# Kernel optimization log

Measured on AMD Instinct MI355X. Metric: run time of the kernel, lower is better.

Reference implementation:

```python
import jax, jax.numpy as jnp
import numpy as np

N = 100_000      # nodes
E = 3_200_000    # directed edges (avg degree 32)
F_IN = 503
C = 32           # GATConv out_channels, heads=1
NEG_SLOPE = 0.2  # PyG GATConv default


def setup_inputs() -> dict:
    key = jax.random.key(0)
    ks = jax.random.split(key, 14)
    x = jax.random.normal(ks[0], (N, F_IN), jnp.float32)
    edge_index = jax.random.randint(ks[1], (2, E), 0, N)
    edge_weight = jax.random.uniform(ks[2], (E, 1), jnp.float32)
    input_mask = jnp.ones((N, 1), jnp.float32)
    # GATConv params (heads=1)
    W_src = jax.random.normal(ks[3], (C, F_IN), jnp.float32) * 0.02
    att_src = jax.random.normal(ks[4], (C,), jnp.float32) * 0.1
    att_dst = jax.random.normal(ks[5], (C,), jnp.float32) * 0.1
    att_edge = jax.random.normal(ks[6], (C,), jnp.float32) * 0.1
    W_edge = jax.random.normal(ks[7], (C, 1), jnp.float32) * 0.1
    bias_conv = jnp.zeros((C,), jnp.float32)
    # dense heads
    Wb = jax.random.normal(ks[8], (1, C), jnp.float32) * 0.1
    bb = jnp.zeros((1,), jnp.float32)
    Ww = jax.random.normal(ks[9], (1, C), jnp.float32) * 0.1
    bw = jnp.zeros((1,), jnp.float32)
    return {"x": x, "edge_index": edge_index, "edge_weight": edge_weight,
            "input_mask": input_mask, "W_src": W_src, "att_src": att_src,
            "att_dst": att_dst, "att_edge": att_edge, "W_edge": W_edge,
            "bias_conv": bias_conv, "Wb": Wb, "bb": bb, "Ww": Ww, "bw": bw}


def reference(x, edge_index, edge_weight, input_mask, W_src, att_src, att_dst,
              att_edge, W_edge, bias_conv, Wb, bb, Ww, bw):
    n = x.shape[0]
    xl = x @ W_src.T                       # [N, C] transformed node features
    a_src = xl @ att_src                   # [N] per-node source attention logit
    a_dst = xl @ att_dst                   # [N]
    src, dst = edge_index[0], edge_index[1]
    # add_self_loops=True with fill_value='mean' for edge_attr (PyG default)
    loop = jnp.arange(n)
    mean_attr = jnp.mean(edge_weight, axis=0, keepdims=True)      # [1,1]
    ea = jnp.concatenate([edge_weight, jnp.broadcast_to(mean_attr, (n, 1))], 0)
    s = jnp.concatenate([src, loop])       # [E+N]
    d = jnp.concatenate([dst, loop])
    a_edge = (ea @ W_edge.T) @ att_edge    # [E+N]
    alpha = jax.nn.leaky_relu(a_src[s] + a_dst[d] + a_edge, NEG_SLOPE)
    # softmax over incoming edges of each destination node
    amax = jax.ops.segment_max(alpha, d, num_segments=n)
    ex = jnp.exp(alpha - amax[d])
    denom = jax.ops.segment_sum(ex, d, num_segments=n)
    w = ex / denom[d]                      # [E+N] attention coeffs
    msg = xl[s] * w[:, None]               # [E+N, C]
    out = jax.ops.segment_sum(msg, d, num_segments=n) + bias_conv  # [N, C]
    h = jax.nn.relu(out)
    biases = (h @ Wb.T + bb) * input_mask  # [N, 1]
    weights = ((h[src] + h[dst]) * 0.5) @ Ww.T + bw  # [E, 1]
    return weights, biases
```

## Files before the change

### kernel.cpp

```cpp
#include <hip/hip_runtime.h>
#include <stdint.h>

#define NN 100000
#define NE 3200000
#define FIN 503
#define COUT 32
#define NSLOPE 0.2f

#define BSH 6
#define NB 1563
#define HB 256
#define EPB (NE / HB)
#define NSB 7
#define MAXBE 2560

typedef __bf16 bf16x8 __attribute__((ext_vector_type(8)));
typedef float  f32x4  __attribute__((ext_vector_type(4)));

__device__ __forceinline__ unsigned short bf1(float f) {
    unsigned u = __float_as_uint(f);
    u = (u + 0x7FFFu + ((u >> 16) & 1u)) >> 16;
    return (unsigned short)u;
}
__device__ __forceinline__ unsigned bf2(float a, float b) {
    return (unsigned)bf1(a) | ((unsigned)bf1(b) << 16);
}
__device__ __forceinline__ float unbf(unsigned short h) {
    return __uint_as_float(((unsigned)h) << 16);
}

__global__ __launch_bounds__(256)
void k_pre(const int* __restrict__ ei_dst, const float* __restrict__ ew,
           const float* __restrict__ W, uint4* __restrict__ wfrag,
           float* __restrict__ partial, unsigned* __restrict__ part,
           unsigned* __restrict__ done)
{
    __shared__ unsigned h[NB];
    __shared__ float wsum[4];
    const int t = threadIdx.x;
    const int b = blockIdx.x;
    const int gid = b * 256 + t;

    if (gid == 0) *done = 0u;
    for (int i = t; i < NB; i += 256) h[i] = 0u;

    if (gid < 2048) {
        int c = gid & 31;
        int quad = (gid >> 5) & 3;
        int chunk = gid >> 7;
        int kb = chunk * 32 + quad * 8;
        float v[8];
        #pragma unroll
        for (int j = 0; j < 8; ++j) {
            int k = kb + j;
            v[j] = (k < FIN) ? W[c * FIN + k] : 0.f;
        }
        uint4 o;
        o.x = bf2(v[0], v[1]); o.y = bf2(v[2], v[3]);
        o.z = bf2(v[4], v[5]); o.w = bf2(v[6], v[7]);
        wfrag[gid] = o;
    }
    __syncthreads();

    const int base = b * EPB;
    for (int i = t; i < EPB; i += 256)
        atomicAdd(&h[ei_dst[base + i] >> BSH], 1u);

    const float4* ew4 = (const float4*)ew;
    float s = 0.f;
    for (int i = gid; i < NE / 4; i += HB * 256) {
        float4 v = ew4[i];
        s += v.x + v.y + v.z + v.w;
    }
    #pragma unroll
    for (int off = 32; off > 0; off >>= 1) s += __shfl_xor(s, off);
    if ((t & 63) == 0) wsum[t >> 6] = s;
    __syncthreads();
    if (t == 0) partial[b] = wsum[0] + wsum[1] + wsum[2] + wsum[3];
    for (int i = t; i < NB; i += 256)
        part[(size_t)b * NB + i] = h[i];
}

#define GR 64

__global__ __launch_bounds__(256)
void k_gemm(const float* __restrict__ x, const uint4* __restrict__ wfrag,
            const float* __restrict__ att_s, const float* __restrict__ att_d,
            unsigned short* __restrict__ xlb,
            float* __restrict__ a_src, float* __restrict__ a_dst)
{
    __shared__ __align__(16) float xs[2][GR][36];
    unsigned short* os = (unsigned short*)&xs[0][0][0];
    const int t = threadIdx.x;
    const int wv = t >> 6, lane = t & 63;
    const int m16 = lane & 15, quad = lane >> 4;
    const int row0 = blockIdx.x * GR;
    const int srow = t >> 5;
    const int scol = t & 31;
    const int rowf = wv * 16 + m16;

    auto stage = [&](int ch, int buf) {
        const int k = ch * 32 + scol;
        const bool ok = (k < FIN);
        #pragma unroll
        for (int p = 0; p < 8; ++p) {
            int r = p * 8 + srow;
            int rg = row0 + r;
            rg = (rg < NN) ? rg : (NN - 1);
            xs[buf][r][scol] = ok ? x[(size_t)rg * FIN + k] : 0.f;
        }
    };

    f32x4 acc0 = {0.f, 0.f, 0.f, 0.f};
    f32x4 acc1 = {0.f, 0.f, 0.f, 0.f};

    stage(0, 0);
    for (int ch = 0; ch < 16; ++ch) {
        __syncthreads();
        if (ch < 15) stage(ch + 1, (ch + 1) & 1);
        float av[8];
        *(f32x4*)&av[0] = *(const f32x4*)&xs[ch & 1][rowf][quad * 8];
        *(f32x4*)&av[4] = *(const f32x4*)&xs[ch & 1][rowf][quad * 8 + 4];
        bf16x8 af;
        #pragma unroll
        for (int j = 0; j < 8; ++j) af[j] = (__bf16)av[j];
        uint4 b0 = wfrag[ch * 128 + quad * 32 + m16];
        uint4 b1 = wfrag[ch * 128 + quad * 32 + 16 + m16];
        acc0 = __builtin_amdgcn_mfma_f32_16x16x32_bf16(af, *(bf16x8*)&b0, acc0, 0, 0, 0);
        acc1 = __builtin_amdgcn_mfma_f32_16x16x32_bf16(af, *(bf16x8*)&b1, acc1, 0, 0, 0);
    }

    #pragma unroll
    for (int r = 0; r < 4; ++r) {
        int rr = wv * 16 + quad * 4 + r;
        os[rr * 40 + m16]      = bf1(acc0[r]);
        os[rr * 40 + 16 + m16] = bf1(acc1[r]);
    }
    __syncthreads();
    {
        int r = t >> 2, c0 = (t & 3) * 8;
        int grow = row0 + r;
        uint4 o = *(const uint4*)&os[r * 40 + c0];
        float s = 0.f, dd = 0.f;
        const unsigned short* oh = (const unsigned short*)&o;
        #pragma unroll
        for (int j = 0; j < 8; ++j) {
            float v = unbf(oh[j]);
            s  += v * att_s[c0 + j];
            dd += v * att_d[c0 + j];
        }
        s  += __shfl_xor(s, 1, 4);  s  += __shfl_xor(s, 2, 4);
        dd += __shfl_xor(dd, 1, 4); dd += __shfl_xor(dd, 2, 4);
        if (grow < NN) {
            *(uint4*)&xlb[(size_t)grow * COUT + c0] = o;
            if ((t & 3) == 0) { a_src[grow] = s; a_dst[grow] = dd; }
        }
    }
}

__global__ __launch_bounds__(256)
void k_scan(unsigned* __restrict__ part, unsigned* __restrict__ colsum,
            unsigned* __restrict__ done, const float* __restrict__ partial,
            const float* __restrict__ W_edge, const float* __restrict__ att_e,
            float* __restrict__ stats, unsigned* __restrict__ bbase)
{
    const int t = threadIdx.x;
    const int bkt = blockIdx.x * 256 + t;
    if (bkt < NB) {
        unsigned run = 0u;
        #pragma unroll 1
        for (int s = 0; s < HB; s += 4) {
            unsigned v0 = part[(size_t)(s    ) * NB + bkt];
            unsigned v1 = part[(size_t)(s + 1) * NB + bkt];
            unsigned v2 = part[(size_t)(s + 2) * NB + bkt];
            unsigned v3 = part[(size_t)(s + 3) * NB + bkt];
            part[(size_t)(s    ) * NB + bkt] = run; run += v0;
            part[(size_t)(s + 1) * NB + bkt] = run; run += v1;
            part[(size_t)(s + 2) * NB + bkt] = run; run += v2;
            part[(size_t)(s + 3) * NB + bkt] = run; run += v3;
        }
        colsum[bkt] = run;
    }
    __threadfence();
    __syncthreads();
    __shared__ unsigned winner;
    if (t == 0) winner = atomicAdd(done, 1u);
    __syncthreads();
    if (winner != NSB - 1) return;

    __shared__ float fs[256];
    fs[t] = partial[t];
    __syncthreads();
    for (int off = 128; off > 0; off >>= 1) {
        if (t < off) fs[t] += fs[t + off];
        __syncthreads();
    }
    if (t == 0) {
        stats[0] = fs[0];
        float k = 0.f;
        for (int c = 0; c < COUT; ++c) k += W_edge[c] * att_e[c];
        stats[1] = k;
    }
    __syncthreads();
    __shared__ unsigned sm[256];
    __shared__ unsigned carry;
    if (t == 0) carry = 0u;
    __syncthreads();
    for (int c0 = 0; c0 < NB; c0 += 256) {
        int i = c0 + t;
        unsigned cv = (i < NB) ? atomicAdd(&colsum[i], 0u) : 0u;
        sm[t] = cv;
        for (int off = 1; off < 256; off <<= 1) {
            __syncthreads();
            unsigned tv = (t >= off) ? sm[t - off] : 0u;
            __syncthreads();
            sm[t] += tv;
        }
        __syncthreads();
        if (i < NB) bbase[i] = carry + sm[t] - cv;
        __syncthreads();
        if (t == 0) carry += sm[255];
        __syncthreads();
    }
    if (t == 0) bbase[NB] = carry;
}

__global__ __launch_bounds__(512)
void k_scatter(const int* __restrict__ ei, const float* __restrict__ ew,
               const float* __restrict__ a_src, const float* __restrict__ stats,
               const unsigned* __restrict__ part, const unsigned* __restrict__ bbase,
               uint2* __restrict__ csr)
{
    __shared__ unsigned cur[NB];
    const int b = blockIdx.x;
    const int t = threadIdx.x;
    for (int i = t; i < NB; i += 512)
        cur[i] = bbase[i] + part[(size_t)b * NB + i];
    __syncthreads();
    const float kc = stats[1];
    const int base = b * EPB;
    for (int i = t; i < EPB; i += 512) {
        int e = base + i;
        int s = ei[e];
        int d = ei[NE + e];
        float pre = a_src[s] + kc * ew[e];
        unsigned pos = atomicAdd(&cur[d >> BSH], 1u);
        csr[pos] = make_uint2((unsigned)s | ((unsigned)(d & 63) << 20),
                              __float_as_uint(pre));
    }
}

__global__ __launch_bounds__(256)
void k_aggr(const uint2* __restrict__ csr, const unsigned* __restrict__ bbase,
            const float* __restrict__ a_src, const float* __restrict__ a_dst,
            const unsigned short* __restrict__ xlb, const float* __restrict__ stats,
            const float* __restrict__ bias_conv, const float* __restrict__ Wb,
            const float* __restrict__ bb, const float* __restrict__ Ww,
            const float* __restrict__ mask, float* __restrict__ out_b,
            float* __restrict__ hw)
{
    __shared__ uint2 rec[MAXBE];
    __shared__ unsigned seg[65], cur[64];
    const int t = threadIdx.x;
    const int b = blockIdx.x;
    const int jb = (int)bbase[b];
    int ne = (int)bbase[b + 1] - jb;
    if (ne > MAXBE) ne = MAXBE;

    if (t < 64) cur[t] = 0u;
    __syncthreads();
    for (int i = t; i < ne; i += 256)
        atomicAdd(&cur[csr[jb + i].x >> 20], 1u);
    __syncthreads();
    if (t < 64) {
        unsigned v = cur[t];
        unsigned s = v;
        #pragma unroll
        for (int off = 1; off < 64; off <<= 1) {
            unsigned u = __shfl_up(s, off, 64);
            if (t >= off) s += u;
        }
        seg[t + 1] = s;
        cur[t] = s - v;
        if (t == 0) seg[0] = 0u;
    }
    __syncthreads();
    for (int i = t; i < ne; i += 256) {
        uint2 r = csr[jb + i];
        unsigned pos = atomicAdd(&cur[r.x >> 20], 1u);
        rec[pos] = r;
    }
    __syncthreads();

    const float kmean = stats[1] * (stats[0] * (1.f / NE));
    const int lane = t & 31;
    for (int dl = t >> 5; dl < 64; dl += 8) {
        int d = (b << BSH) + dl;
        if (d >= NN) continue;
        const float adv = a_dst[d];
        float a0 = a_src[d] + adv + kmean;
        a0 = (a0 > 0.f) ? a0 : NSLOPE * a0;
        const float ps = __expf(a0);
        float l = 0.f;
        float acc = ps * unbf(xlb[(size_t)d * COUT + lane]);
        const int j0 = (int)seg[dl], j1 = (int)seg[dl + 1];
        for (int tb = j0; tb < j1; tb += 32) {
            int j = tb + lane;
            float p = 0.f;
            if (j < j1) {
                uint2 en = rec[j];
                float a = __uint_as_float(en.y) + adv;
                a = (a > 0.f) ? a : NSLOPE * a;
                p = __expf(a);
                rec[j].y = __float_as_uint(p);
            }
            l += p;
            int cnte = min(32, j1 - tb);
            #pragma unroll 4
            for (int k = 0; k < cnte; ++k) {
                uint2 en = rec[tb + k];
                acc += __uint_as_float(en.y) *
                       unbf(xlb[(size_t)(en.x & 0xFFFFFu) * COUT + lane]);
            }
        }
        #pragma unroll
        for (int off = 16; off > 0; off >>= 1) l += __shfl_xor(l, off, 32);
        l += ps;
        float h = fmaxf(acc / l + bias_conv[lane], 0.f);
        float pb = h * Wb[lane];
        float pw = h * Ww[lane];
        #pragma unroll
        for (int off = 16; off > 0; off >>= 1) {
            pb += __shfl_xor(pb, off, 32);
            pw += __shfl_xor(pw, off, 32);
        }
        if (lane == 0) {
            out_b[d] = (pb + bb[0]) * mask[d];
            hw[d] = pw;
        }
    }
}

__global__ void k_weights(const int* __restrict__ ei, const float* __restrict__ hw,
                          const float* __restrict__ bw, float* __restrict__ out_w)
{
    int e4 = blockIdx.x * 256 + threadIdx.x;
    if (e4 < NE / 4) {
        int4 s4 = ((const int4*)ei)[e4];
        int4 d4 = ((const int4*)(ei + NE))[e4];
        float bwv = bw[0];
        float4 o;
        o.x = 0.5f * (hw[s4.x] + hw[d4.x]) + bwv;
        o.y = 0.5f * (hw[s4.y] + hw[d4.y]) + bwv;
        o.z = 0.5f * (hw[s4.z] + hw[d4.z]) + bwv;
        o.w = 0.5f * (hw[s4.w] + hw[d4.w]) + bwv;
        ((float4*)out_w)[e4] = o;
    }
}

extern "C" void kernel_launch(void* const* d_in, const int* in_sizes, int n_in,
                              void* d_out, int out_size, void* d_ws, size_t ws_size,
                              hipStream_t stream)
{
    const float* x        = (const float*)d_in[0];
    const int*   ei       = (const int*)d_in[1];
    const float* ew       = (const float*)d_in[2];
    const float* mask     = (const float*)d_in[3];
    const float* W_src    = (const float*)d_in[4];
    const float* att_src  = (const float*)d_in[5];
    const float* att_dst  = (const float*)d_in[6];
    const float* att_edge = (const float*)d_in[7];
    const float* W_edge   = (const float*)d_in[8];
    const float* bias_c   = (const float*)d_in[9];
    const float* Wb       = (const float*)d_in[10];
    const float* bb       = (const float*)d_in[11];
    const float* Ww       = (const float*)d_in[12];
    const float* bw       = (const float*)d_in[13];
    (void)in_sizes; (void)n_in; (void)out_size; (void)ws_size;

    char* wsp = (char*)d_ws;
    size_t off = 0;
    auto alloc = [&](size_t bytes) -> void* {
        void* p = wsp + off;
        off = (off + bytes + 255) & ~(size_t)255;
        return p;
    };
    unsigned short* xlb    = (unsigned short*)alloc((size_t)NN * COUT * 2);
    uint4*    wfrag  = (uint4*)alloc(2048 * 16);
    float*    a_src  = (float*)alloc((size_t)NN * 4);
    float*    a_dst  = (float*)alloc((size_t)NN * 4);
    float*    stats  = (float*)alloc(256);
    float*    partial= (float*)alloc((size_t)HB * 4);
    unsigned* part   = (unsigned*)alloc((size_t)HB * NB * 4);
    unsigned* colsum = (unsigned*)alloc((size_t)NB * 4);
    unsigned* bbase  = (unsigned*)alloc((size_t)(NB + 1) * 4);
    unsigned* done   = (unsigned*)alloc(256);
    uint2*    csr    = (uint2*)alloc((size_t)NE * 8);
    float*    hw     = (float*)alloc((size_t)NN * 4);

    float* out_w = (float*)d_out;
    float* out_b = out_w + NE;

    k_pre     <<<HB, 256, 0, stream>>>(ei + NE, ew, W_src, wfrag, partial, part, done);
    k_gemm    <<<(NN + GR - 1) / GR, 256, 0, stream>>>(x, wfrag, att_src, att_dst,
                                                       xlb, a_src, a_dst);
    k_scan    <<<NSB, 256, 0, stream>>>(part, colsum, done, partial, W_edge,
                                        att_edge, stats, bbase);
    k_scatter <<<HB, 512, 0, stream>>>(ei, ew, a_src, stats, part, bbase, csr);
    k_aggr    <<<NB, 256, 0, stream>>>(csr, bbase, a_src, a_dst, xlb, stats,
                                       bias_c, Wb, bb, Ww, mask, out_b, hw);
    k_weights <<<NE / 4 / 256, 256, 0, stream>>>(ei, hw, bw, out_w);
}
```

Measured before the change: 561.9 us.

## Fuse histogram prepass into GEMM kernel and widen histogram partitioning

Merges the histogram/edge-weight-sum prepass and the feature GEMM into one launch: the first blocks do the GEMM, loading W rows directly from global memory and converting them to bf16, while the extra blocks build per-block destination histograms. This drops a kernel launch and the wfrag staging buffer, and lets the histogram work overlap with the GEMM. The histogram/scatter partition count is doubled to 512 blocks of 256 threads, which doubles the size of the scan's partial-count array and the per-block bucket initialisation cost in the scatter kernel. Each GEMM wave now issues strided per-element loads of W instead of reading pre-packed fragments.

Result: slower. 573.5 us (+2.0%).

```diff
diff --git a/kernel.cpp b/kernel.cpp
--- a/kernel.cpp
+++ b/kernel.cpp
@@ -9,8 +9,9 @@
 
 #define BSH 6
 #define NB 1563
-#define HB 256
-#define EPB (NE / HB)
+#define NGB 1563
+#define NHB 512
+#define EPB (NE / NHB)
 #define NSB 7
 #define MAXBE 2560
 
@@ -22,82 +23,59 @@
     u = (u + 0x7FFFu + ((u >> 16) & 1u)) >> 16;
     return (unsigned short)u;
 }
-__device__ __forceinline__ unsigned bf2(float a, float b) {
-    return (unsigned)bf1(a) | ((unsigned)bf1(b) << 16);
-}
 __device__ __forceinline__ float unbf(unsigned short h) {
     return __uint_as_float(((unsigned)h) << 16);
 }
 
+#define GR 64
+
 __global__ __launch_bounds__(256)
-void k_pre(const int* __restrict__ ei_dst, const float* __restrict__ ew,
-           const float* __restrict__ W, uint4* __restrict__ wfrag,
-           float* __restrict__ partial, unsigned* __restrict__ part,
-           unsigned* __restrict__ done)
-{
-    __shared__ unsigned h[NB];
-    __shared__ float wsum[4];
+void k_fused1(const float* __restrict__ x, const float* __restrict__ W,
+              const float* __restrict__ att_s, const float* __restrict__ att_d,
+              unsigned short* __restrict__ xlb,
+              float* __restrict__ a_src, float* __restrict__ a_dst,
+              const int* __restrict__ ei_dst, const float* __restrict__ ew,
+              float* __restrict__ partial, unsigned* __restrict__ part,
+              unsigned* __restrict__ done)
+{
+    __shared__ __align__(16) float xs[2][GR][36];
     const int t = threadIdx.x;
-    const int b = blockIdx.x;
-    const int gid = b * 256 + t;
-
-    if (gid == 0) *done = 0u;
-    for (int i = t; i < NB; i += 256) h[i] = 0u;
-
-    if (gid < 2048) {
-        int c = gid & 31;
-        int quad = (gid >> 5) & 3;
-        int chunk = gid >> 7;
-        int kb = chunk * 32 + quad * 8;
-        float v[8];
-        #pragma unroll
-        for (int j = 0; j < 8; ++j) {
-            int k = kb + j;
-            v[j] = (k < FIN) ? W[c * FIN + k] : 0.f;
-        }
-        uint4 o;
-        o.x = bf2(v[0], v[1]); o.y = bf2(v[2], v[3]);
-        o.z = bf2(v[4], v[5]); o.w = bf2(v[6], v[7]);
-        wfrag[gid] = o;
-    }
-    __syncthreads();
-
-    const int base = b * EPB;
-    for (int i = t; i < EPB; i += 256)
-        atomicAdd(&h[ei_dst[base + i] >> BSH], 1u);
-
-    const float4* ew4 = (const float4*)ew;
-    float s = 0.f;
-    for (int i = gid; i < NE / 4; i += HB * 256) {
-        float4 v = ew4[i];
-        s += v.x + v.y + v.z + v.w;
-    }
-    #pragma unroll
-    for (int off = 32; off > 0; off >>= 1) s += __shfl_xor(s, off);
-    if ((t & 63) == 0) wsum[t >> 6] = s;
-    __syncthreads();
-    if (t == 0) partial[b] = wsum[0] + wsum[1] + wsum[2] + wsum[3];
-    for (int i = t; i < NB; i += 256)
-        part[(size_t)b * NB + i] = h[i];
-}
-
-#define GR 64
-
-__global__ __launch_bounds__(256)
-void k_gemm(const float* __restrict__ x, const uint4* __restrict__ wfrag,
-            const float* __restrict__ att_s, const float* __restrict__ att_d,
-            unsigned short* __restrict__ xlb,
-            float* __restrict__ a_src, float* __restrict__ a_dst)
-{
-    __shared__ __align__(16) float xs[2][GR][36];
+
+    if (blockIdx.x >= NGB) {
+        unsigned* h = (unsigned*)&xs[0][0][0];
+        __shared__ float wsum[4];
+        const int hb = blockIdx.x - NGB;
+        for (int i = t; i < NB; i += 256) h[i] = 0u;
+        __syncthreads();
+        const int base = hb * EPB;
+        for (int i = t; i < EPB; i += 256)
+            atomicAdd(&h[ei_dst[base + i] >> BSH], 1u);
+        const float4* ew4 = (const float4*)ew;
+        float s = 0.f;
+        for (int i = hb * 256 + t; i < NE / 4; i += NHB * 256) {
+            float4 v = ew4[i];
+            s += v.x + v.y + v.z + v.w;
+        }
+        #pragma unroll
+        for (int off = 32; off > 0; off >>= 1) s += __shfl_xor(s, off);
+        if ((t & 63) == 0) wsum[t >> 6] = s;
+        __syncthreads();
+        if (t == 0) partial[hb] = wsum[0] + wsum[1] + wsum[2] + wsum[3];
+        for (int i = t; i < NB; i += 256)
+            part[(size_t)hb * NB + i] = h[i];
+        return;
+    }
+
+    if (blockIdx.x == 0 && t == 0) *done = 0u;
     unsigned short* os = (unsigned short*)&xs[0][0][0];
-    const int t = threadIdx.x;
     const int wv = t >> 6, lane = t & 63;
     const int m16 = lane & 15, quad = lane >> 4;
     const int row0 = blockIdx.x * GR;
     const int srow = t >> 5;
     const int scol = t & 31;
     const int rowf = wv * 16 + m16;
+    const float* wr0 = W + (size_t)m16 * FIN;
+    const float* wr1 = W + (size_t)(m16 + 16) * FIN;
 
     auto stage = [&](int ch, int buf) {
         const int k = ch * 32 + scol;
@@ -118,16 +96,29 @@
     for (int ch = 0; ch < 16; ++ch) {
         __syncthreads();
         if (ch < 15) stage(ch + 1, (ch + 1) & 1);
+        const int kb = ch * 32 + quad * 8;
         float av[8];
         *(f32x4*)&av[0] = *(const f32x4*)&xs[ch & 1][rowf][quad * 8];
         *(f32x4*)&av[4] = *(const f32x4*)&xs[ch & 1][rowf][quad * 8 + 4];
-        bf16x8 af;
-        #pragma unroll
-        for (int j = 0; j < 8; ++j) af[j] = (__bf16)av[j];
-        uint4 b0 = wfrag[ch * 128 + quad * 32 + m16];
-        uint4 b1 = wfrag[ch * 128 + quad * 32 + 16 + m16];
-        acc0 = __builtin_amdgcn_mfma_f32_16x16x32_bf16(af, *(bf16x8*)&b0, acc0, 0, 0, 0);
-        acc1 = __builtin_amdgcn_mfma_f32_16x16x32_bf16(af, *(bf16x8*)&b1, acc1, 0, 0, 0);
+        bf16x8 af, b0f, b1f;
+        if (ch < 15) {
+            #pragma unroll
+            for (int j = 0; j < 8; ++j) {
+                af[j]  = (__bf16)av[j];
+                b0f[j] = (__bf16)wr0[kb + j];
+                b1f[j] = (__bf16)wr1[kb + j];
+            }
+        } else {
+            #pragma unroll
+            for (int j = 0; j < 8; ++j) {
+                af[j]  = (__bf16)av[j];
+                bool ok = (kb + j < FIN);
+                b0f[j] = (__bf16)(ok ? wr0[kb + j] : 0.f);
+                b1f[j] = (__bf16)(ok ? wr1[kb + j] : 0.f);
+            }
+        }
+        acc0 = __builtin_amdgcn_mfma_f32_16x16x32_bf16(af, b0f, acc0, 0, 0, 0);
+        acc1 = __builtin_amdgcn_mfma_f32_16x16x32_bf16(af, b1f, acc1, 0, 0, 0);
     }
 
     #pragma unroll
@@ -169,15 +160,15 @@
     if (bkt < NB) {
         unsigned run = 0u;
         #pragma unroll 1
-        for (int s = 0; s < HB; s += 4) {
-            unsigned v0 = part[(size_t)(s    ) * NB + bkt];
-            unsigned v1 = part[(size_t)(s + 1) * NB + bkt];
-            unsigned v2 = part[(size_t)(s + 2) * NB + bkt];
-            unsigned v3 = part[(size_t)(s + 3) * NB + bkt];
-            part[(size_t)(s    ) * NB + bkt] = run; run += v0;
-            part[(size_t)(s + 1) * NB + bkt] = run; run += v1;
-            part[(size_t)(s + 2) * NB + bkt] = run; run += v2;
-            part[(size_t)(s + 3) * NB + bkt] = run; run += v3;
+        for (int s = 0; s < NHB; s += 8) {
+            unsigned v[8];
+            #pragma unroll
+            for (int j = 0; j < 8; ++j) v[j] = part[(size_t)(s + j) * NB + bkt];
+            #pragma unroll
+            for (int j = 0; j < 8; ++j) {
+                part[(size_t)(s + j) * NB + bkt] = run;
+                run += v[j];
+            }
         }
         colsum[bkt] = run;
     }
@@ -189,7 +180,7 @@
     if (winner != NSB - 1) return;
 
     __shared__ float fs[256];
-    fs[t] = partial[t];
+    fs[t] = partial[t] + partial[t + 256];
     __syncthreads();
     for (int off = 128; off > 0; off >>= 1) {
         if (t < off) fs[t] += fs[t + off];
@@ -225,7 +216,7 @@
     if (t == 0) bbase[NB] = carry;
 }
 
-__global__ __launch_bounds__(512)
+__global__ __launch_bounds__(256)
 void k_scatter(const int* __restrict__ ei, const float* __restrict__ ew,
                const float* __restrict__ a_src, const float* __restrict__ stats,
                const unsigned* __restrict__ part, const unsigned* __restrict__ bbase,
@@ -234,12 +225,12 @@
     __shared__ unsigned cur[NB];
     const int b = blockIdx.x;
     const int t = threadIdx.x;
-    for (int i = t; i < NB; i += 512)
+    for (int i = t; i < NB; i += 256)
         cur[i] = bbase[i] + part[(size_t)b * NB + i];
     __syncthreads();
     const float kc = stats[1];
     const int base = b * EPB;
-    for (int i = t; i < EPB; i += 512) {
+    for (int i = t; i < EPB; i += 256) {
         int e = base + i;
         int s = ei[e];
         int d = ei[NE + e];
@@ -386,12 +377,11 @@
         return p;
     };
     unsigned short* xlb    = (unsigned short*)alloc((size_t)NN * COUT * 2);
-    uint4*    wfrag  = (uint4*)alloc(2048 * 16);
     float*    a_src  = (float*)alloc((size_t)NN * 4);
     float*    a_dst  = (float*)alloc((size_t)NN * 4);
     float*    stats  = (float*)alloc(256);
-    float*    partial= (float*)alloc((size_t)HB * 4);
-    unsigned* part   = (unsigned*)alloc((size_t)HB * NB * 4);
+    float*    partial= (float*)alloc((size_t)NHB * 4);
+    unsigned* part   = (unsigned*)alloc((size_t)NHB * NB * 4);
     unsigned* colsum = (unsigned*)alloc((size_t)NB * 4);
     unsigned* bbase  = (unsigned*)alloc((size_t)(NB + 1) * 4);
     unsigned* done   = (unsigned*)alloc(256);
@@ -401,12 +391,12 @@
     float* out_w = (float*)d_out;
     float* out_b = out_w + NE;
 
-    k_pre     <<<HB, 256, 0, stream>>>(ei + NE, ew, W_src, wfrag, partial, part, done);
-    k_gemm    <<<(NN + GR - 1) / GR, 256, 0, stream>>>(x, wfrag, att_src, att_dst,
-                                                       xlb, a_src, a_dst);
+    k_fused1  <<<NGB + NHB, 256, 0, stream>>>(x, W_src, att_src, att_dst,
+                                              xlb, a_src, a_dst,
+                                              ei + NE, ew, partial, part, done);
     k_scan    <<<NSB, 256, 0, stream>>>(part, colsum, done, partial, W_edge,
                                         att_edge, stats, bbase);
-    k_scatter <<<HB, 512, 0, stream>>>(ei, ew, a_src, stats, part, bbase, csr);
+    k_scatter <<<NHB, 256, 0, stream>>>(ei, ew, a_src, stats, part, bbase, csr);
     k_aggr    <<<NB, 256, 0, stream>>>(csr, bbase, a_src, a_dst, xlb, stats,
                                        bias_c, Wb, bb, Ww, mask, out_b, hw);
     k_weights <<<NE / 4 / 256, 256, 0, stream>>>(ei, hw, bw, out_w);
```

## Split histogram out of preprocessing and drop double-buffering in GEMM

Applied to the files above, without the earlier changes.

The combined pre-kernel is split in two. A 1024-block stats kernel handles the edge-weight sum and the W fragment packing, and a separate 512-thread histogram kernel builds the per-block destination bucket counts after the GEMM. The scan kernel now folds 1024 partial sums instead of 256. The GEMM kernel drops its double-buffered shared-memory staging for a single buffer with two barriers per chunk, which lowers LDS use but removes load/compute overlap.

New measurement: 548.4 us. 2.4% less time.

```diff
diff --git a/kernel.cpp b/kernel.cpp
--- a/kernel.cpp
+++ b/kernel.cpp
@@ -30,19 +30,13 @@
 }
 
 __global__ __launch_bounds__(256)
-void k_pre(const int* __restrict__ ei_dst, const float* __restrict__ ew,
-           const float* __restrict__ W, uint4* __restrict__ wfrag,
-           float* __restrict__ partial, unsigned* __restrict__ part,
-           unsigned* __restrict__ done)
-{
-    __shared__ unsigned h[NB];
-    __shared__ float wsum[4];
+void k_stats(const float* __restrict__ ew, float* __restrict__ partial,
+             const float* __restrict__ W, uint4* __restrict__ wfrag,
+             unsigned* __restrict__ done)
+{
     const int t = threadIdx.x;
-    const int b = blockIdx.x;
-    const int gid = b * 256 + t;
-
+    const int gid = blockIdx.x * 256 + t;
     if (gid == 0) *done = 0u;
-    for (int i = t; i < NB; i += 256) h[i] = 0u;
 
     if (gid < 2048) {
         int c = gid & 31;
@@ -60,25 +54,19 @@
         o.z = bf2(v[4], v[5]); o.w = bf2(v[6], v[7]);
         wfrag[gid] = o;
     }
-    __syncthreads();
-
-    const int base = b * EPB;
-    for (int i = t; i < EPB; i += 256)
-        atomicAdd(&h[ei_dst[base + i] >> BSH], 1u);
 
     const float4* ew4 = (const float4*)ew;
     float s = 0.f;
-    for (int i = gid; i < NE / 4; i += HB * 256) {
+    for (int i = gid; i < NE / 4; i += gridDim.x * 256) {
         float4 v = ew4[i];
         s += v.x + v.y + v.z + v.w;
     }
     #pragma unroll
     for (int off = 32; off > 0; off >>= 1) s += __shfl_xor(s, off);
+    __shared__ float wsum[4];
     if ((t & 63) == 0) wsum[t >> 6] = s;
     __syncthreads();
-    if (t == 0) partial[b] = wsum[0] + wsum[1] + wsum[2] + wsum[3];
-    for (int i = t; i < NB; i += 256)
-        part[(size_t)b * NB + i] = h[i];
+    if (t == 0) partial[blockIdx.x] = wsum[0] + wsum[1] + wsum[2] + wsum[3];
 }
 
 #define GR 64
@@ -89,38 +77,32 @@
             unsigned short* __restrict__ xlb,
             float* __restrict__ a_src, float* __restrict__ a_dst)
 {
-    __shared__ __align__(16) float xs[2][GR][36];
-    unsigned short* os = (unsigned short*)&xs[0][0][0];
+    __shared__ __align__(16) float xs[GR][36];
+    __shared__ __align__(16) unsigned short os[GR * 40];
     const int t = threadIdx.x;
     const int wv = t >> 6, lane = t & 63;
     const int m16 = lane & 15, quad = lane >> 4;
     const int row0 = blockIdx.x * GR;
     const int srow = t >> 5;
     const int scol = t & 31;
+
+    f32x4 acc0 = {0.f, 0.f, 0.f, 0.f};
+    f32x4 acc1 = {0.f, 0.f, 0.f, 0.f};
     const int rowf = wv * 16 + m16;
 
-    auto stage = [&](int ch, int buf) {
+    for (int ch = 0; ch < 16; ++ch) {
         const int k = ch * 32 + scol;
-        const bool ok = (k < FIN);
         #pragma unroll
         for (int p = 0; p < 8; ++p) {
             int r = p * 8 + srow;
             int rg = row0 + r;
             rg = (rg < NN) ? rg : (NN - 1);
-            xs[buf][r][scol] = ok ? x[(size_t)rg * FIN + k] : 0.f;
-        }
-    };
-
-    f32x4 acc0 = {0.f, 0.f, 0.f, 0.f};
-    f32x4 acc1 = {0.f, 0.f, 0.f, 0.f};
-
-    stage(0, 0);
-    for (int ch = 0; ch < 16; ++ch) {
-        __syncthreads();
-        if (ch < 15) stage(ch + 1, (ch + 1) & 1);
+            xs[r][scol] = (k < FIN) ? x[(size_t)rg * FIN + k] : 0.f;
+        }
+        __syncthreads();
         float av[8];
-        *(f32x4*)&av[0] = *(const f32x4*)&xs[ch & 1][rowf][quad * 8];
-        *(f32x4*)&av[4] = *(const f32x4*)&xs[ch & 1][rowf][quad * 8 + 4];
+        *(f32x4*)&av[0] = *(const f32x4*)&xs[rowf][quad * 8];
+        *(f32x4*)&av[4] = *(const f32x4*)&xs[rowf][quad * 8 + 4];
         bf16x8 af;
         #pragma unroll
         for (int j = 0; j < 8; ++j) af[j] = (__bf16)av[j];
@@ -128,6 +110,7 @@
         uint4 b1 = wfrag[ch * 128 + quad * 32 + 16 + m16];
         acc0 = __builtin_amdgcn_mfma_f32_16x16x32_bf16(af, *(bf16x8*)&b0, acc0, 0, 0, 0);
         acc1 = __builtin_amdgcn_mfma_f32_16x16x32_bf16(af, *(bf16x8*)&b1, acc1, 0, 0, 0);
+        __syncthreads();
     }
 
     #pragma unroll
@@ -156,6 +139,20 @@
             if ((t & 3) == 0) { a_src[grow] = s; a_dst[grow] = dd; }
         }
     }
+}
+
+__global__ __launch_bounds__(512)
+void k_hist(const int* __restrict__ ei_dst, unsigned* __restrict__ part)
+{
+    __shared__ unsigned h[NB];
+    for (int i = threadIdx.x; i < NB; i += 512) h[i] = 0u;
+    __syncthreads();
+    const int base = blockIdx.x * EPB;
+    for (int i = threadIdx.x; i < EPB; i += 512)
+        atomicAdd(&h[ei_dst[base + i] >> BSH], 1u);
+    __syncthreads();
+    for (int i = threadIdx.x; i < NB; i += 512)
+        part[(size_t)blockIdx.x * NB + i] = h[i];
 }
 
 __global__ __launch_bounds__(256)
@@ -189,7 +186,7 @@
     if (winner != NSB - 1) return;
 
     __shared__ float fs[256];
-    fs[t] = partial[t];
+    fs[t] = partial[t] + partial[t + 256] + partial[t + 512] + partial[t + 768];
     __syncthreads();
     for (int off = 128; off > 0; off >>= 1) {
         if (t < off) fs[t] += fs[t + off];
@@ -233,13 +230,12 @@
 {
     __shared__ unsigned cur[NB];
     const int b = blockIdx.x;
-    const int t = threadIdx.x;
-    for (int i = t; i < NB; i += 512)
+    for (int i = threadIdx.x; i < NB; i += 512)
         cur[i] = bbase[i] + part[(size_t)b * NB + i];
     __syncthreads();
     const float kc = stats[1];
     const int base = b * EPB;
-    for (int i = t; i < EPB; i += 512) {
+    for (int i = threadIdx.x; i < EPB; i += 512) {
         int e = base + i;
         int s = ei[e];
         int d = ei[NE + e];
@@ -390,7 +386,7 @@
     float*    a_src  = (float*)alloc((size_t)NN * 4);
     float*    a_dst  = (float*)alloc((size_t)NN * 4);
     float*    stats  = (float*)alloc(256);
-    float*    partial= (float*)alloc((size_t)HB * 4);
+    float*    partial= (float*)alloc(1024 * 4);
     unsigned* part   = (unsigned*)alloc((size_t)HB * NB * 4);
     unsigned* colsum = (unsigned*)alloc((size_t)NB * 4);
     unsigned* bbase  = (unsigned*)alloc((size_t)(NB + 1) * 4);
@@ -401,9 +397,10 @@
     float* out_w = (float*)d_out;
     float* out_b = out_w + NE;
 
-    k_pre     <<<HB, 256, 0, stream>>>(ei + NE, ew, W_src, wfrag, partial, part, done);
+    k_stats   <<<1024, 256, 0, stream>>>(ew, partial, W_src, wfrag, done);
     k_gemm    <<<(NN + GR - 1) / GR, 256, 0, stream>>>(x, wfrag, att_src, att_dst,
                                                        xlb, a_src, a_dst);
+    k_hist    <<<HB, 512, 0, stream>>>(ei + NE, part);
     k_scan    <<<NSB, 256, 0, stream>>>(part, colsum, done, partial, W_edge,
                                         att_edge, stats, bbase);
     k_scatter <<<HB, 512, 0, stream>>>(ei, ew, a_src, stats, part, bbase, csr);
```
